# Kernel tuning notes

Hardware: AMD Instinct MI355X
Metric: run time of the kernel (lower is better)

The kernel has to match this reference:

```python
import jax, jax.numpy as jnp
import numpy as np

N, M = 32768, 12          # atoms, neighbors
ORIG, NBR, AF, HF = 92, 41, 64, 128
N_CONV = 3
ATOMS_PER = 32            # atoms per crystal
B = N // ATOMS_PER        # number of crystals
EPS = 1e-5                # BatchNorm eps


def softplus(x):
    return jnp.logaddexp(x, 0.0)


def setup_inputs() -> dict:
    key = jax.random.key(0)
    ks = jax.random.split(key, 24)
    s = 0.05
    return {
        "atom_fea": jax.random.normal(ks[0], (N, ORIG), jnp.float32),
        "nbr_fea": jax.random.normal(ks[1], (N, M, NBR), jnp.float32),
        "nbr_fea_idx": jax.random.randint(ks[2], (N, M), 0, N),
        "crystal_id": jnp.arange(N, dtype=jnp.int32) // ATOMS_PER,
        # embedding: Linear(ORIG -> AF)
        "emb_W": jax.random.normal(ks[3], (ORIG, AF), jnp.float32) * s,
        "emb_b": jnp.zeros((AF,), jnp.float32),
        # per-conv-layer params, stacked over N_CONV
        "conv_W": jax.random.normal(ks[4], (N_CONV, 2 * AF + NBR, 2 * AF), jnp.float32) * s,
        "conv_b": jnp.zeros((N_CONV, 2 * AF), jnp.float32),
        "bn1_g": jnp.ones((N_CONV, 2 * AF), jnp.float32),
        "bn1_b": jnp.zeros((N_CONV, 2 * AF), jnp.float32),
        "bn2_g": jnp.ones((N_CONV, AF), jnp.float32),
        "bn2_b": jnp.zeros((N_CONV, AF), jnp.float32),
        # head: conv_to_fc (AF->HF), fcs[0] (HF->HF), fc_out (HF->1)
        "fc1_W": jax.random.normal(ks[5], (AF, HF), jnp.float32) * s,
        "fc1_b": jnp.zeros((HF,), jnp.float32),
        "fc2_W": jax.random.normal(ks[6], (HF, HF), jnp.float32) * s,
        "fc2_b": jnp.zeros((HF,), jnp.float32),
        "out_W": jax.random.normal(ks[7], (HF, 1), jnp.float32) * s,
        "out_b": jnp.zeros((1,), jnp.float32),
    }


def _batchnorm(x, g, b):
    # training-mode BN over the batch (row) axis, biased variance like torch
    mu = x.mean(axis=0)
    var = x.var(axis=0)
    return (x - mu) * jax.lax.rsqrt(var + EPS) * g + b


def reference(atom_fea, nbr_fea, nbr_fea_idx, crystal_id,
              emb_W, emb_b, conv_W, conv_b, bn1_g, bn1_b, bn2_g, bn2_b,
              fc1_W, fc1_b, fc2_W, fc2_b, out_W, out_b):
    x = atom_fea @ emb_W + emb_b                              # (N, AF)
    for l in range(N_CONV):
        nbr_atom = x[nbr_fea_idx]                             # gather (N, M, AF)
        self_fea = jnp.broadcast_to(x[:, None, :], (N, M, AF))
        tot = jnp.concatenate([self_fea, nbr_atom, nbr_fea], axis=2)  # (N,M,2AF+NBR)
        g = tot @ conv_W[l] + conv_b[l]                       # (N, M, 2AF)
        g = _batchnorm(g.reshape(N * M, 2 * AF), bn1_g[l], bn1_b[l]).reshape(N, M, 2 * AF)
        nbr_filter = jax.nn.sigmoid(g[..., :AF])
        nbr_core = softplus(g[..., AF:])
        summed = jnp.sum(nbr_filter * nbr_core, axis=1)       # (N, AF)
        summed = _batchnorm(summed, bn2_g[l], bn2_b[l])
        x = softplus(x + summed)
    # mean pooling per crystal (equal-size crystals of ATOMS_PER atoms)
    pool = jax.ops.segment_sum(x, crystal_id, num_segments=B) / ATOMS_PER  # (B, AF)
    # seq2: softplus -> conv_to_fc -> dropout(p=0) -> softplus -> Linear -> softplus -> dropout(p=0)
    h = softplus(pool)
    h = softplus(h @ fc1_W + fc1_b)
    h = softplus(h @ fc2_W + fc2_b)
    return h @ out_W + out_b                                  # (B, 1)
```

## Files before the change

kernel.cpp:

```cpp
#include <hip/hip_runtime.h>
#include <cmath>

#define DEV __device__ __forceinline__

constexpr int NA    = 32768;
constexpr int M     = 12;
constexpr int ORIG  = 92;
constexpr int NBR   = 41;
constexpr int AF    = 64;
constexpr int C2    = 128;
constexpr int HF    = 128;
constexpr int NCONV = 3;
constexpr int NM    = NA * M;
constexpr int BB    = 1024;
constexpr int TA    = 4;
constexpr int RT    = TA * M;
constexpr int NTILES = NA / TA;
constexpr int GRID_CONV = 4096;
constexpr int TSTRIDE = GRID_CONV / 2;
constexpr int GRID_APPLY = 2048;
constexpr int WLD2  = 68;
constexpr int ALD   = 44;

DEV float fsig(float x) { return __builtin_amdgcn_rcpf(1.f + __expf(-x)); }
DEV float fsp (float x) { return fmaxf(x, 0.f) + __logf(1.f + __expf(-fabsf(x))); }

DEV void fma4(float4& a, float s, const float4 w) {
    a.x = fmaf(s, w.x, a.x); a.y = fmaf(s, w.y, a.y);
    a.z = fmaf(s, w.z, a.z); a.w = fmaf(s, w.w, a.w);
}
DEV void fma2(float2& a, float s, const float2 w) {
    a.x = fmaf(s, w.x, a.x); a.y = fmaf(s, w.y, a.y);
}
DEV float comp4(const float4 v, int i) { return i == 0 ? v.x : i == 1 ? v.y : i == 2 ? v.z : v.w; }
DEV void add2(float2& a, const float2 b) { a.x += b.x; a.y += b.y; }
DEV void sqa2(float2& a, const float2 b) { a.x = fmaf(b.x, b.x, a.x); a.y = fmaf(b.y, b.y, a.y); }
DEV float2 shxor2(const float2 v, int m) {
    float2 r; r.x = __shfl_xor(v.x, m, 64); r.y = __shfl_xor(v.y, m, 64); return r;
}
DEV void bfly2(float2& v) {
    float2 t = shxor2(v, 16); add2(v, t);
    t = shxor2(v, 32); add2(v, t);
}
DEV unsigned bf16pair(float a, float b) {
    unsigned ua = __float_as_uint(a), ub = __float_as_uint(b);
    ua += 0x7fffu + ((ua >> 16) & 1u);
    ub += 0x7fffu + ((ub >> 16) & 1u);
    return (ua >> 16) | (ub & 0xffff0000u);
}
DEV float2 up2(unsigned u) {
    float2 r;
    r.x = __uint_as_float(u << 16);
    r.y = __uint_as_float(u & 0xffff0000u);
    return r;
}

template<bool FIRST>
__global__ __launch_bounds__(256, 4)
void spx_kernel(const float* __restrict__ xin,
                const float* __restrict__ summed,
                const float* __restrict__ ss2,
                const float* __restrict__ atom_fea,
                const float* __restrict__ embW,
                const float* __restrict__ embb,
                const float* __restrict__ W,
                const float* __restrict__ bias,
                float* __restrict__ xout,
                float* __restrict__ S,
                unsigned* __restrict__ Pb)
{
    __shared__ float xs[16][AF];
    __shared__ float af[FIRST ? 16 * ORIG : 4];

    const int a0 = blockIdx.x * 16, tid = threadIdx.x;

    if (FIRST) {
        for (int i = tid; i < 16 * ORIG; i += 256) af[i] = atom_fea[(size_t)a0 * ORIG + i];
        __syncthreads();
        const int row = tid >> 4, c4 = (tid & 15) * 4;
        float4 acc = *(const float4*)(embb + c4);
        #pragma unroll 4
        for (int k = 0; k < ORIG; ++k)
            fma4(acc, af[row * ORIG + k], *(const float4*)(embW + k * AF + c4));
        *(float4*)&xs[row][c4] = acc;
        *(float4*)(xout + (size_t)(a0 + row) * AF + c4) = acc;
    } else {
        const int row = tid >> 4, c4 = (tid & 15) * 4;
        const size_t o = (size_t)(a0 + row) * AF + c4;
        const float4 xi = *(const float4*)(xin + o);
        const float4 sm = *(const float4*)(summed + o);
        const float4 sc = *(const float4*)(ss2 + c4);
        const float4 sh = *(const float4*)(ss2 + AF + c4);
        float4 ov;
        ov.x = fsp(xi.x + fmaf(sm.x, sc.x, sh.x));
        ov.y = fsp(xi.y + fmaf(sm.y, sc.y, sh.y));
        ov.z = fsp(xi.z + fmaf(sm.z, sc.z, sh.z));
        ov.w = fsp(xi.w + fmaf(sm.w, sc.w, sh.w));
        *(float4*)&xs[row][c4] = ov;
        *(float4*)(xout + o) = ov;
    }
    __syncthreads();

    const int cid = tid & 31, rid = tid >> 5;
    const int c0 = cid * 8, r0 = rid * 2;
    const bool isS = (c0 < 128);
    const int cc = c0 & 127;
    const float* Wb = W + (isS ? 0 : AF * C2) + cc;
    float4 a00, a01, a10, a11;
    if (isS) { a00 = *(const float4*)(bias + cc); a01 = *(const float4*)(bias + cc + 4); }
    else     { a00 = {0,0,0,0}; a01 = {0,0,0,0}; }
    a10 = a00; a11 = a01;
    for (int k = 0; k < AF; ++k) {
        const float4 w0 = *(const float4*)(Wb + k * C2);
        const float4 w1 = *(const float4*)(Wb + k * C2 + 4);
        const float x0 = xs[r0][k], x1 = xs[r0 + 1][k];
        fma4(a00, x0, w0); fma4(a01, x0, w1);
        fma4(a10, x1, w0); fma4(a11, x1, w1);
    }
    if (isS) {
        *(float4*)(S + (size_t)(a0 + r0) * C2 + cc)     = a00;
        *(float4*)(S + (size_t)(a0 + r0) * C2 + cc + 4) = a01;
        *(float4*)(S + (size_t)(a0 + r0 + 1) * C2 + cc)     = a10;
        *(float4*)(S + (size_t)(a0 + r0 + 1) * C2 + cc + 4) = a11;
    } else {
        uint4 u0, u1;
        u0.x = bf16pair(a00.x, a00.y); u0.y = bf16pair(a00.z, a00.w);
        u0.z = bf16pair(a01.x, a01.y); u0.w = bf16pair(a01.z, a01.w);
        u1.x = bf16pair(a10.x, a10.y); u1.y = bf16pair(a10.z, a10.w);
        u1.z = bf16pair(a11.x, a11.y); u1.w = bf16pair(a11.z, a11.w);
        *(uint4*)(Pb + (size_t)(a0 + r0) * 64 + cc / 2)     = u0;
        *(uint4*)(Pb + (size_t)(a0 + r0 + 1) * 64 + cc / 2) = u1;
    }
}

__global__ __launch_bounds__(256, 4)
void conv8_kernel(const float* __restrict__ nbr_fea,
                  const int* __restrict__ idx,
                  const float* __restrict__ W2,
                  const float* __restrict__ S,
                  const unsigned* __restrict__ Pb,
                  float* __restrict__ P1s, float* __restrict__ P1q,
                  unsigned* __restrict__ gout)
{
    __shared__ float W2h[NBR * WLD2];
    __shared__ float sA[RT * ALD];

    const int tid  = threadIdx.x;
    const int cid  = tid & 15;
    const int rid  = tid >> 4;
    const int ch   = blockIdx.x & 1;
    const int c2   = cid * 2;
    const int gf   = ch * 32 + c2;
    const int gc   = 64 + gf;
    const int r0   = rid * 3;
    const int atom = tid >> 6;

    for (int i = tid; i < NBR * 16; i += 256) {
        const int k = i >> 4, q = i & 15;
        const int srcc = (q < 8) ? (ch * 32 + q * 4) : (64 + ch * 32 + (q - 8) * 4);
        *(float4*)&W2h[k * WLD2 + q * 4] = *(const float4*)(W2 + k * C2 + srcc);
    }

    int soff[8];
    #pragma unroll
    for (int i = 0; i < 8; ++i) {
        const int e = tid + 256 * i;
        if (e < RT * NBR) {
            const int r = (int)(((unsigned)e * 102301u) >> 22);
            soff[i] = r * ALD + (e - r * NBR);
        } else soff[i] = -1;
    }

    float2 sum_f = {0,0}, sum_c = {0,0}, sq_f = {0,0}, sq_c = {0,0};

    for (int t = blockIdx.x >> 1; t < NTILES; t += TSTRIDE) {
        const int n0 = t * TA;
        const int ib = n0 * M + r0;
        const int j0 = idx[ib + 0];
        const int j1 = idx[ib + 1];
        const int j2 = idx[ib + 2];
        const unsigned u0f = Pb[(size_t)j0 * 64 + ch * 16 + cid];
        const unsigned u0c = Pb[(size_t)j0 * 64 + 32 + ch * 16 + cid];
        const unsigned u1f = Pb[(size_t)j1 * 64 + ch * 16 + cid];
        const unsigned u1c = Pb[(size_t)j1 * 64 + 32 + ch * 16 + cid];
        const unsigned u2f = Pb[(size_t)j2 * 64 + ch * 16 + cid];
        const unsigned u2c = Pb[(size_t)j2 * 64 + 32 + ch * 16 + cid];
        const float2 svf = *(const float2*)(S + (size_t)(n0 + atom) * C2 + gf);
        const float2 svc = *(const float2*)(S + (size_t)(n0 + atom) * C2 + gc);

        __syncthreads();
        {
            const float* src = nbr_fea + (size_t)n0 * M * NBR;
            #pragma unroll
            for (int i = 0; i < 8; ++i) if (soff[i] >= 0) sA[soff[i]] = src[tid + 256 * i];
        }
        __syncthreads();

        float2 ef0 = svf, ec0 = svc, ef1 = svf, ec1 = svc, ef2 = svf, ec2 = svc;
        add2(ef0, up2(u0f)); add2(ec0, up2(u0c));
        add2(ef1, up2(u1f)); add2(ec1, up2(u1c));
        add2(ef2, up2(u2f)); add2(ec2, up2(u2c));

        const float4* A0 = (const float4*)(sA + (r0 + 0) * ALD);
        const float4* A1 = (const float4*)(sA + (r0 + 1) * ALD);
        const float4* A2 = (const float4*)(sA + (r0 + 2) * ALD);
        #pragma unroll 2
        for (int k4 = 0; k4 < 10; ++k4) {
            const float4 a0 = A0[k4], a1 = A1[k4], a2 = A2[k4];
            #pragma unroll
            for (int kk = 0; kk < 4; ++kk) {
                const int k = 4 * k4 + kk;
                const float2 wf = *(const float2*)(W2h + k * WLD2 + c2);
                const float2 wc = *(const float2*)(W2h + k * WLD2 + 32 + c2);
                fma2(ef0, comp4(a0, kk), wf); fma2(ec0, comp4(a0, kk), wc);
                fma2(ef1, comp4(a1, kk), wf); fma2(ec1, comp4(a1, kk), wc);
                fma2(ef2, comp4(a2, kk), wf); fma2(ec2, comp4(a2, kk), wc);
            }
        }
        {
            const float2 wf = *(const float2*)(W2h + 40 * WLD2 + c2);
            const float2 wc = *(const float2*)(W2h + 40 * WLD2 + 32 + c2);
            const float a0s = sA[(r0 + 0) * ALD + 40];
            const float a1s = sA[(r0 + 1) * ALD + 40];
            const float a2s = sA[(r0 + 2) * ALD + 40];
            fma2(ef0, a0s, wf); fma2(ec0, a0s, wc);
            fma2(ef1, a1s, wf); fma2(ec1, a1s, wc);
            fma2(ef2, a2s, wf); fma2(ec2, a2s, wc);
        }

        {
            const size_t row0 = (size_t)(n0 * M + r0) * 64 + ch * 16 + cid;
            gout[row0]       = bf16pair(ef0.x, ef0.y);
            gout[row0 + 32]  = bf16pair(ec0.x, ec0.y);
            gout[row0 + 64]  = bf16pair(ef1.x, ef1.y);
            gout[row0 + 96]  = bf16pair(ec1.x, ec1.y);
            gout[row0 + 128] = bf16pair(ef2.x, ef2.y);
            gout[row0 + 160] = bf16pair(ec2.x, ec2.y);
        }

        add2(sum_f, ef0); add2(sum_f, ef1); add2(sum_f, ef2);
        add2(sum_c, ec0); add2(sum_c, ec1); add2(sum_c, ec2);
        sqa2(sq_f, ef0);  sqa2(sq_f, ef1);  sqa2(sq_f, ef2);
        sqa2(sq_c, ec0);  sqa2(sq_c, ec1);  sqa2(sq_c, ec2);
    }

    bfly2(sum_f); bfly2(sum_c); bfly2(sq_f); bfly2(sq_c);
    __syncthreads();
    if ((tid & 48) == 0) {
        *(float2*)&sA[atom * 64 + c2]            = sum_f;
        *(float2*)&sA[atom * 64 + 32 + c2]       = sum_c;
        *(float2*)&sA[256 + atom * 64 + c2]      = sq_f;
        *(float2*)&sA[256 + atom * 64 + 32 + c2] = sq_c;
    }
    __syncthreads();
    if (tid < 64) {
        P1s[(size_t)blockIdx.x * 64 + tid] = sA[tid] + sA[64 + tid] + sA[128 + tid] + sA[192 + tid];
        P1q[(size_t)blockIdx.x * 64 + tid] = sA[256 + tid] + sA[256 + 64 + tid]
                                           + sA[256 + 128 + tid] + sA[256 + 192 + tid];
    }
}

__global__ __launch_bounds__(256)
void apply_g_kernel(const unsigned* __restrict__ g,
                    const float* __restrict__ ss1,
                    float* __restrict__ summed,
                    float* __restrict__ P2s, float* __restrict__ P2q)
{
    const int tid = threadIdx.x;
    const int al  = tid >> 5;
    const int c2  = tid & 31;
    const int cA  = 2 * c2;
    const float2 scf = *(const float2*)(ss1 + cA);
    const float2 scc = *(const float2*)(ss1 + 64 + cA);
    const float2 shf = *(const float2*)(ss1 + C2 + cA);
    const float2 shc = *(const float2*)(ss1 + C2 + 64 + cA);
    float2 ts = {0.f, 0.f}, tq = {0.f, 0.f};

    for (int grp = blockIdx.x; grp < NA / 8; grp += gridDim.x) {
        const int a = grp * 8 + al;
        const unsigned* gr = g + (size_t)a * M * 64 + c2;
        float2 acc = {0.f, 0.f};
        #pragma unroll
        for (int m = 0; m < M; ++m) {
            const unsigned uf = gr[m * 64];
            const unsigned us = gr[m * 64 + 32];
            const float2 f = up2(uf);
            const float2 s = up2(us);
            acc.x = fmaf(fsig(fmaf(f.x, scf.x, shf.x)), fsp(fmaf(s.x, scc.x, shc.x)), acc.x);
            acc.y = fmaf(fsig(fmaf(f.y, scf.y, shf.y)), fsp(fmaf(s.y, scc.y, shc.y)), acc.y);
        }
        *(float2*)(summed + (size_t)a * AF + cA) = acc;
        ts.x += acc.x; ts.y += acc.y;
        tq.x = fmaf(acc.x, acc.x, tq.x); tq.y = fmaf(acc.y, acc.y, tq.y);
    }

    __shared__ float2 rs[8][32], rq[8][32];
    rs[al][c2] = ts; rq[al][c2] = tq;
    __syncthreads();
    if (tid < 32) {
        float2 s = rs[0][tid], q = rq[0][tid];
        #pragma unroll
        for (int a = 1; a < 8; ++a) {
            s.x += rs[a][tid].x; s.y += rs[a][tid].y;
            q.x += rq[a][tid].x; q.y += rq[a][tid].y;
        }
        *(float2*)(P2s + (size_t)blockIdx.x * AF + 2 * tid) = s;
        *(float2*)(P2q + (size_t)blockIdx.x * AF + 2 * tid) = q;
    }
}

__global__ __launch_bounds__(256)
void bn_finalize_half(const float* __restrict__ Ps, const float* __restrict__ Pq,
                      int rowlen, float invn,
                      const float* __restrict__ gamma, const float* __restrict__ beta,
                      float* __restrict__ ss, int Ctot)
{
    __shared__ float sd[256];
    const int c = blockIdx.x, tid = threadIdx.x;
    const int ch = (c >> 5) & 1;
    const int lc = (c & 31) + ((c >= 64) ? 32 : 0);
    float s = 0.f;
    for (int i = tid; i < TSTRIDE; i += 256) s += Ps[(size_t)(ch + 2 * i) * rowlen + lc];
    sd[tid] = s; __syncthreads();
    for (int st = 128; st > 0; st >>= 1) { if (tid < st) sd[tid] += sd[tid + st]; __syncthreads(); }
    const float total = sd[0];
    __syncthreads();
    float q = 0.f;
    for (int i = tid; i < TSTRIDE; i += 256) q += Pq[(size_t)(ch + 2 * i) * rowlen + lc];
    sd[tid] = q; __syncthreads();
    for (int st = 128; st > 0; st >>= 1) { if (tid < st) sd[tid] += sd[tid + st]; __syncthreads(); }
    if (tid == 0) {
        const float mean = total * invn;
        const float var  = sd[0] * invn - mean * mean;
        const float scl  = gamma[c] * rsqrtf(var + 1e-5f);
        ss[c]        = scl;
        ss[Ctot + c] = beta[c] - mean * scl;
    }
}

__global__ __launch_bounds__(256)
void bn_finalize_plain(const float* __restrict__ Ps, const float* __restrict__ Pq,
                       int npart, int C, float invn,
                       const float* __restrict__ gamma, const float* __restrict__ beta,
                       float* __restrict__ ss)
{
    __shared__ float sd[256];
    const int c = blockIdx.x, tid = threadIdx.x;
    float s = 0.f;
    for (int j = tid; j < npart; j += 256) s += Ps[(size_t)j * C + c];
    sd[tid] = s; __syncthreads();
    for (int st = 128; st > 0; st >>= 1) { if (tid < st) sd[tid] += sd[tid + st]; __syncthreads(); }
    const float total = sd[0];
    __syncthreads();
    float q = 0.f;
    for (int j = tid; j < npart; j += 256) q += Pq[(size_t)j * C + c];
    sd[tid] = q; __syncthreads();
    for (int st = 128; st > 0; st >>= 1) { if (tid < st) sd[tid] += sd[tid + st]; __syncthreads(); }
    if (tid == 0) {
        const float mean = total * invn;
        const float var  = sd[0] * invn - mean * mean;
        const float scl  = gamma[c] * rsqrtf(var + 1e-5f);
        ss[c]     = scl;
        ss[C + c] = beta[c] - mean * scl;
    }
}

__global__ __launch_bounds__(128)
void head_kernel(const float* __restrict__ x,
                 const float* __restrict__ summed,
                 const float* __restrict__ ss2,
                 const float* __restrict__ fc1W, const float* __restrict__ fc1b,
                 const float* __restrict__ fc2W, const float* __restrict__ fc2b,
                 const float* __restrict__ outW, const float* __restrict__ outb,
                 float* __restrict__ out)
{
    __shared__ float l0[AF], l1[HF], rr[2], hs[2][AF];
    const int b = blockIdx.x, tid = threadIdx.x;
    const int col = tid & 63, half = tid >> 6;
    {
        const float sc = ss2[col], sh = ss2[AF + col];
        float s = 0.f;
        #pragma unroll 4
        for (int a = half * 16; a < half * 16 + 16; ++a) {
            const size_t o = (size_t)(b * 32 + a) * AF + col;
            s += fsp(x[o] + fmaf(summed[o], sc, sh));
        }
        hs[half][col] = s;
    }
    __syncthreads();
    if (tid < AF) l0[tid] = fsp((hs[0][tid] + hs[1][tid]) * (1.f / 32.f));
    __syncthreads();
    float acc = fc1b[tid];
    #pragma unroll 4
    for (int k = 0; k < AF; ++k) acc = fmaf(l0[k], fc1W[k * HF + tid], acc);
    l1[tid] = fsp(acc);
    __syncthreads();
    acc = fc2b[tid];
    #pragma unroll 4
    for (int k = 0; k < HF; ++k) acc = fmaf(l1[k], fc2W[k * HF + tid], acc);
    float v = fsp(acc) * outW[tid];
    #pragma unroll
    for (int off = 32; off > 0; off >>= 1) v += __shfl_down(v, off, 64);
    if ((tid & 63) == 0) rr[tid >> 6] = v;
    __syncthreads();
    if (tid == 0) out[b] = rr[0] + rr[1] + outb[0];
}

extern "C" void kernel_launch(void* const* d_in, const int* in_sizes, int n_in,
                              void* d_out, int out_size, void* d_ws, size_t ws_size,
                              hipStream_t stream)
{
    const float* atom_fea = (const float*)d_in[0];
    const float* nbr_fea  = (const float*)d_in[1];
    const int*   nbr_idx  = (const int*)d_in[2];
    const float* emb_W  = (const float*)d_in[4];
    const float* emb_b  = (const float*)d_in[5];
    const float* conv_W = (const float*)d_in[6];
    const float* conv_b = (const float*)d_in[7];
    const float* bn1_g  = (const float*)d_in[8];
    const float* bn1_b  = (const float*)d_in[9];
    const float* bn2_g  = (const float*)d_in[10];
    const float* bn2_b  = (const float*)d_in[11];
    const float* fc1W   = (const float*)d_in[12];
    const float* fc1b   = (const float*)d_in[13];
    const float* fc2W   = (const float*)d_in[14];
    const float* fc2b   = (const float*)d_in[15];
    const float* outW   = (const float*)d_in[16];
    const float* outb   = (const float*)d_in[17];
    float* out = (float*)d_out;
    float* ws  = (float*)d_ws;

    float*    x_a    = ws;
    float*    x_b    = x_a + (size_t)NA * AF;
    float*    Sbuf   = x_b + (size_t)NA * AF;
    unsigned* Pb     = (unsigned*)(Sbuf + (size_t)NA * C2);
    float*    summed = (float*)(Pb + (size_t)NA * 64);
    float*    P1s    = summed + (size_t)NA * AF;
    float*    P1q    = P1s + (size_t)GRID_CONV * 64;
    float*    P2s    = P1q + (size_t)GRID_CONV * 64;
    float*    P2q    = P2s + (size_t)GRID_APPLY * AF;
    float*    ss1    = P2q + (size_t)GRID_APPLY * AF;
    float*    ss2    = ss1 + 2 * C2;
    unsigned* gbuf   = (unsigned*)(ss2 + 2 * AF);

    float* xcur = x_a;
    spx_kernel<true><<<NA / 16, 256, 0, stream>>>(nullptr, nullptr, nullptr,
                                                  atom_fea, emb_W, emb_b,
                                                  conv_W, conv_b, xcur, Sbuf, Pb);
    for (int l = 0; l < NCONV; ++l) {
        const float* W2 = conv_W + (size_t)l * (C2 + NBR) * C2 + (size_t)C2 * C2;
        conv8_kernel<<<GRID_CONV, 256, 0, stream>>>(nbr_fea, nbr_idx, W2,
                                                    Sbuf, Pb, P1s, P1q, gbuf);
        bn_finalize_half<<<C2, 256, 0, stream>>>(P1s, P1q, 64, 1.f / (float)NM,
                                                 bn1_g + l * C2, bn1_b + l * C2, ss1, C2);
        apply_g_kernel<<<GRID_APPLY, 256, 0, stream>>>(gbuf, ss1, summed, P2s, P2q);
        bn_finalize_plain<<<AF, 256, 0, stream>>>(P2s, P2q, GRID_APPLY, AF, 1.f / (float)NA,
                                                  bn2_g + l * AF, bn2_b + l * AF, ss2);
        if (l < NCONV - 1) {
            float* xnext = (xcur == x_a) ? x_b : x_a;
            spx_kernel<false><<<NA / 16, 256, 0, stream>>>(xcur, summed, ss2,
                                                           nullptr, nullptr, nullptr,
                                                           conv_W + (size_t)(l + 1) * (C2 + NBR) * C2,
                                                           conv_b + (size_t)(l + 1) * C2,
                                                           xnext, Sbuf, Pb);
            xcur = xnext;
        }
    }
    head_kernel<<<BB, 128, 0, stream>>>(xcur, summed, ss2,
                                        fc1W, fc1b, fc2W, fc2b, outW, outb, out);
}
```

Measured before the change: 701.4 us.

## Software-pipeline conv8 tile loads into registers and raise occupancy hint

```diff
diff --git a/kernel.cpp b/kernel.cpp
--- a/kernel.cpp
+++ b/kernel.cpp
@@ -133,7 +133,7 @@
     }
 }
 
-__global__ __launch_bounds__(256, 4)
+__global__ __launch_bounds__(256, 5)
 void conv8_kernel(const float* __restrict__ nbr_fea,
                   const int* __restrict__ idx,
                   const float* __restrict__ W2,
@@ -155,6 +155,23 @@
     const int r0   = rid * 3;
     const int atom = tid >> 6;
 
+    const int q0 = blockIdx.x >> 1;
+
+    int j0, j1, j2;
+    float2 svf, svc;
+    float st[8];
+    {
+        const int n0 = q0 * TA;
+        const int ib = n0 * M + r0;
+        j0 = idx[ib]; j1 = idx[ib + 1]; j2 = idx[ib + 2];
+        svf = *(const float2*)(S + (size_t)(n0 + atom) * C2 + gf);
+        svc = *(const float2*)(S + (size_t)(n0 + atom) * C2 + gc);
+        const float* src = nbr_fea + (size_t)n0 * M * NBR;
+        #pragma unroll
+        for (int i = 0; i < 8; ++i)
+            if (tid + 256 * i < RT * NBR) st[i] = src[tid + 256 * i];
+    }
+
     for (int i = tid; i < NBR * 16; i += 256) {
         const int k = i >> 4, q = i & 15;
         const int srcc = (q < 8) ? (ch * 32 + q * 4) : (64 + ch * 32 + (q - 8) * 4);
@@ -173,34 +190,37 @@
 
     float2 sum_f = {0,0}, sum_c = {0,0}, sq_f = {0,0}, sq_c = {0,0};
 
-    for (int t = blockIdx.x >> 1; t < NTILES; t += TSTRIDE) {
+    for (int it = 0; it < 4; ++it) {
+        const int t  = q0 + it * TSTRIDE;
         const int n0 = t * TA;
-        const int ib = n0 * M + r0;
-        const int j0 = idx[ib + 0];
-        const int j1 = idx[ib + 1];
-        const int j2 = idx[ib + 2];
+
         const unsigned u0f = Pb[(size_t)j0 * 64 + ch * 16 + cid];
         const unsigned u0c = Pb[(size_t)j0 * 64 + 32 + ch * 16 + cid];
         const unsigned u1f = Pb[(size_t)j1 * 64 + ch * 16 + cid];
         const unsigned u1c = Pb[(size_t)j1 * 64 + 32 + ch * 16 + cid];
         const unsigned u2f = Pb[(size_t)j2 * 64 + ch * 16 + cid];
         const unsigned u2c = Pb[(size_t)j2 * 64 + 32 + ch * 16 + cid];
-        const float2 svf = *(const float2*)(S + (size_t)(n0 + atom) * C2 + gf);
-        const float2 svc = *(const float2*)(S + (size_t)(n0 + atom) * C2 + gc);
+
+        const float2 cf = svf, cc = svc;
 
         __syncthreads();
-        {
-            const float* src = nbr_fea + (size_t)n0 * M * NBR;
+        #pragma unroll
+        for (int i = 0; i < 8; ++i) if (soff[i] >= 0) sA[soff[i]] = st[i];
+        __syncthreads();
+
+        if (it < 3) {
+            const int nn0 = (t + TSTRIDE) * TA;
+            const int ib = nn0 * M + r0;
+            j0 = idx[ib]; j1 = idx[ib + 1]; j2 = idx[ib + 2];
+            svf = *(const float2*)(S + (size_t)(nn0 + atom) * C2 + gf);
+            svc = *(const float2*)(S + (size_t)(nn0 + atom) * C2 + gc);
+            const float* src = nbr_fea + (size_t)nn0 * M * NBR;
             #pragma unroll
-            for (int i = 0; i < 8; ++i) if (soff[i] >= 0) sA[soff[i]] = src[tid + 256 * i];
-        }
-        __syncthreads();
-
-        float2 ef0 = svf, ec0 = svc, ef1 = svf, ec1 = svc, ef2 = svf, ec2 = svc;
-        add2(ef0, up2(u0f)); add2(ec0, up2(u0c));
-        add2(ef1, up2(u1f)); add2(ec1, up2(u1c));
-        add2(ef2, up2(u2f)); add2(ec2, up2(u2c));
-
+            for (int i = 0; i < 8; ++i)
+                if (tid + 256 * i < RT * NBR) st[i] = src[tid + 256 * i];
+        }
+
+        float2 ef0 = {0,0}, ec0 = {0,0}, ef1 = {0,0}, ec1 = {0,0}, ef2 = {0,0}, ec2 = {0,0};
         const float4* A0 = (const float4*)(sA + (r0 + 0) * ALD);
         const float4* A1 = (const float4*)(sA + (r0 + 1) * ALD);
         const float4* A2 = (const float4*)(sA + (r0 + 2) * ALD);
@@ -227,6 +247,13 @@
             fma2(ef1, a1s, wf); fma2(ec1, a1s, wc);
             fma2(ef2, a2s, wf); fma2(ec2, a2s, wc);
         }
+
+        add2(ef0, cf); add2(ef0, up2(u0f));
+        add2(ec0, cc); add2(ec0, up2(u0c));
+        add2(ef1, cf); add2(ef1, up2(u1f));
+        add2(ec1, cc); add2(ec1, up2(u1c));
+        add2(ef2, cf); add2(ef2, up2(u2f));
+        add2(ec2, cc); add2(ec2, up2(u2c));
 
         {
             const size_t row0 = (size_t)(n0 * M + r0) * 64 + ch * 16 + cid;
```

Measured after the change: 677.6 us. 1.04x faster.
